# Kernel tuning notes

Measured on AMD Instinct MI355X. Metric: run time of the kernel, lower is better.

The kernel has to match this reference:

```python
import jax, jax.numpy as jnp
import numpy as np

HIDDEN = 1024
HEADS = 16
HEAD_DIM = HIDDEN // HEADS
SCALE = float(np.sqrt(HEAD_DIM))
B, S = 4, 2048


def setup_inputs() -> dict:
    key = jax.random.key(0)
    ks = jax.random.split(key, 10)
    inp = {
        "query": jax.random.normal(ks[0], (B, S, HIDDEN), dtype=jnp.float32),
        "mask": jax.random.randint(ks[1], (B, S), 0, 2).astype(jnp.bool_),
        "Wq": jax.random.normal(ks[2], (HIDDEN, HIDDEN), dtype=jnp.float32) * 0.02,
        "bq": jax.random.normal(ks[3], (HIDDEN,), dtype=jnp.float32) * 0.02,
        "Wk": jax.random.normal(ks[4], (HIDDEN, HIDDEN), dtype=jnp.float32) * 0.02,
        "bk": jax.random.normal(ks[5], (HIDDEN,), dtype=jnp.float32) * 0.02,
        "Wv": jax.random.normal(ks[6], (HIDDEN, HIDDEN), dtype=jnp.float32) * 0.02,
        "bv": jax.random.normal(ks[7], (HIDDEN,), dtype=jnp.float32) * 0.02,
        "Wo": jax.random.normal(ks[8], (HIDDEN, HIDDEN), dtype=jnp.float32) * 0.02,
        "bo": jax.random.normal(ks[9], (HIDDEN,), dtype=jnp.float32) * 0.02,
    }
    return inp


def reference(query, mask, Wq, bq, Wk, bk, Wv, bv, Wo, bo):
    b, s, _ = query.shape
    # QKV projections (torch Linear: x @ W.T + b)
    q = query @ Wq.T + bq
    k = query @ Wk.T + bk
    v = query @ Wv.T + bv
    # [b, h, s, d]
    q = q.reshape(b, s, HEADS, HEAD_DIM).transpose(0, 2, 1, 3)
    k = k.reshape(b, s, HEADS, HEAD_DIM).transpose(0, 2, 1, 3)
    v = v.reshape(b, s, HEADS, HEAD_DIM).transpose(0, 2, 1, 3)
    # energy[b,h,i,j] = q_i . k_j / scale
    energy = jnp.einsum("bhid,bhjd->bhij", q, k) / SCALE
    m = mask.astype(energy.dtype)
    energy = energy * m[:, None, :, None] * m[:, None, None, :]
    # NOTE: softmax over the QUERY axis (dim=2), not the key axis
    attention = jax.nn.softmax(energy, axis=2)
    x = jnp.einsum("bhij,bhjd->bhid", attention, v)
    x = x.transpose(0, 2, 1, 3).reshape(b, s, HIDDEN)
    out = x @ Wo.T + bo
    return jnp.squeeze(out)
```

## Files before the change

### kernel.cpp

```cpp
#include <hip/hip_runtime.h>

#define SQ   2048
#define HIDN 1024
#define NB   4
#define NH   16
#define HD   64

typedef __attribute__((ext_vector_type(8))) short short8;
typedef __attribute__((ext_vector_type(4))) short short4v;
typedef __attribute__((ext_vector_type(4))) float f32x4;

__device__ __forceinline__ short f2bf(float f) {
  union { float f; unsigned u; } x; x.f = f;
  unsigned r = (x.u + 0x7fffu + ((x.u >> 16) & 1u)) >> 16;
  return (short)r;
}

__device__ __forceinline__ unsigned cvtpk_bf16(float lo, float hi) {
  unsigned u;
  asm("v_cvt_pk_bf16_f32 %0, %1, %2" : "=v"(u) : "v"(lo), "v"(hi));
  return u;
}

__device__ __forceinline__ float exp2_raw(float x) {
  float r;
  asm("v_exp_f32 %0, %1" : "=v"(r) : "v"(x));
  return r;
}

#define MFMA(a, b, c) __builtin_amdgcn_mfma_f32_16x16x32_bf16((a), (b), (c), 0, 0, 0)

__device__ __forceinline__ void gload16(const void* g, void* l) {
  __builtin_amdgcn_global_load_lds(
      (const __attribute__((address_space(1))) unsigned*)g,
      (__attribute__((address_space(3))) unsigned*)l, 16, 0, 0);
}

#define LOG2E 1.44269504f

__global__ __launch_bounds__(256) void k_maskprep(const unsigned* __restrict__ mraw,
                                                  float* __restrict__ m) {
  __shared__ unsigned red[256];
  const int tid = threadIdx.x;
  unsigned w_or = 0;
  for (int i = tid; i < 2048; i += 256) w_or |= mraw[i];
  red[tid] = w_or;
  __syncthreads();
  for (int s = 128; s > 0; s >>= 1) {
    if (tid < s) red[tid] |= red[tid + s];
    __syncthreads();
  }
  const unsigned allw = red[0];
  int mode;
  if ((allw & 0xFFFFFFFEu) == 0) mode = 0;
  else if ((allw & 0xFEFEFEFEu) == 0) mode = 1;
  else mode = 2;
  const unsigned char* mb = (const unsigned char*)mraw;
  const float* mf = (const float*)mraw;
  const int* mi = (const int*)mraw;
  for (int i = tid; i < NB * SQ; i += 256) {
    float v;
    if (mode == 0)      v = mi[i] ? 1.0f : 0.0f;
    else if (mode == 1) v = mb[i] ? 1.0f : 0.0f;
    else                v = (mf[i] != 0.0f) ? 1.0f : 0.0f;
    m[i] = v;
  }
}

__global__ __launch_bounds__(256) void k_cvt(
    const float* __restrict__ query, const float* __restrict__ Wq,
    const float* __restrict__ Wk, const float* __restrict__ Wv,
    short* __restrict__ qbf, short* __restrict__ wbf)
{
  const int yy = blockIdx.y;
  const float* __restrict__ src = (yy == 0) ? query : (yy == 1) ? Wq : (yy == 2) ? Wk : Wv;
  short* __restrict__ dst = (yy == 0) ? qbf : wbf + (yy - 1) * (HIDN * HIDN);
  const int n = (yy == 0) ? (NB * SQ * HIDN) : (HIDN * HIDN);
  const int i = (blockIdx.x * 256 + threadIdx.x) * 4;
  if (i >= n) return;
  const f32x4 v = *(const f32x4*)(src + i);
  short4v s;
#pragma unroll
  for (int e = 0; e < 4; ++e) s[e] = f2bf(v[e]);
  *(short4v*)(dst + i) = s;
}

__global__ __launch_bounds__(256) void k_cvtWo(
    const float* __restrict__ Wo, short* __restrict__ wo)
{
  const int i = (blockIdx.x * 256 + threadIdx.x) * 4;
  if (i >= HIDN * HIDN) return;
  const f32x4 v = *(const f32x4*)(Wo + i);
  short4v s;
#pragma unroll
  for (int e = 0; e < 4; ++e) s[e] = f2bf(v[e]);
  *(short4v*)(wo + i) = s;
}

__global__ __launch_bounds__(256) void k_proj_qkv2(
    const short* __restrict__ qbf, const short* __restrict__ wbf,
    const float* __restrict__ bq, const float* __restrict__ bkb,
    const float* __restrict__ bv, const float* __restrict__ mfl,
    short* __restrict__ qh, short* __restrict__ kh, short* __restrict__ vh)
{
  __shared__ short a_s[2][128 * 64];
  __shared__ short b_s[2][128 * 64];
  const int nt = blockIdx.x, mt = blockIdx.y;
  const int tid = threadIdx.x;
  const int w = tid >> 6, lane = tid & 63;
  const int wr = w >> 1, wc = w & 1;
  const int lg = lane >> 4, lr = lane & 15;

  const int z = nt >> 3;
  const float* __restrict__ bias = (z == 0) ? bq : (z == 1) ? bkb : bv;

  int srow[4], scs[4], sbase[4];
#pragma unroll
  for (int p = 0; p < 4; ++p) {
    const int id = p * 256 + tid;
    const int r = id >> 3, c = id & 7;
    srow[p] = r;
    scs[p] = c ^ (r & 7);
    sbase[p] = (p * 256 + w * 64) * 8;
  }

  f32x4 acc[4][4] = {};

#pragma unroll
  for (int p = 0; p < 4; ++p) {
    gload16(qbf + (size_t)(mt * 128 + srow[p]) * HIDN + scs[p] * 8, a_s[0] + sbase[p]);
    gload16(wbf + (size_t)(nt * 128 + srow[p]) * HIDN + scs[p] * 8, b_s[0] + sbase[p]);
  }
  __syncthreads();

  int cur = 0;
  for (int k0 = 0; k0 < HIDN; k0 += 64) {
    if (k0 + 64 < HIDN) {
      const int kn = k0 + 64;
#pragma unroll
      for (int p = 0; p < 4; ++p) {
        gload16(qbf + (size_t)(mt * 128 + srow[p]) * HIDN + kn + scs[p] * 8,
                a_s[cur ^ 1] + sbase[p]);
        gload16(wbf + (size_t)(nt * 128 + srow[p]) * HIDN + kn + scs[p] * 8,
                b_s[cur ^ 1] + sbase[p]);
      }
    }
#pragma unroll
    for (int kk = 0; kk < 2; ++kk) {
      short8 af[4], bfv[4];
#pragma unroll
      for (int mi = 0; mi < 4; ++mi) {
        const int r = wr * 64 + mi * 16 + lr;
        const int phys = (kk * 4 + lg) ^ (r & 7);
        af[mi] = *(const short8*)((const char*)a_s[cur] + r * 128 + phys * 16);
      }
#pragma unroll
      for (int ni = 0; ni < 4; ++ni) {
        const int r = wc * 64 + ni * 16 + lr;
        const int phys = (kk * 4 + lg) ^ (r & 7);
        bfv[ni] = *(const short8*)((const char*)b_s[cur] + r * 128 + phys * 16);
      }
#pragma unroll
      for (int mi = 0; mi < 4; ++mi)
#pragma unroll
        for (int ni = 0; ni < 4; ++ni)
          acc[mi][ni] = MFMA(af[mi], bfv[ni], acc[mi][ni]);
    }
    __syncthreads();
    cur ^= 1;
  }

#pragma unroll
  for (int mi = 0; mi < 4; ++mi)
#pragma unroll
    for (int ni = 0; ni < 4; ++ni)
#pragma unroll
      for (int r = 0; r < 4; ++r) {
        const int row = mt * 128 + wr * 64 + mi * 16 + lg * 4 + r;
        const int colz = (nt & 7) * 128 + wc * 64 + ni * 16 + lr;
        const float v = acc[mi][ni][r] + bias[colz];
        const int bi = row >> 11, s = row & (SQ - 1);
        const int h = colz >> 6, d = colz & (HD - 1);
        const int idx = ((bi * NH + h) * SQ + s) * HD + d;
        if (z == 0) {
          qh[idx] = f2bf(v * (0.125f * LOG2E) * mfl[row]);
        } else if (z == 1) {
          kh[idx] = f2bf(v * mfl[row]);
        } else {
          vh[idx] = f2bf(v);
        }
      }
}

__global__ __launch_bounds__(256) void k_sumexp_m(
    const short* __restrict__ qh, const short* __restrict__ kh,
    const short* __restrict__ vh, short* __restrict__ vT)
{
  __shared__ short q_s[2][64][72];
  __shared__ float rl_s[256];
  __shared__ short t_s[64][72];
  const int bh = blockIdx.y;
  const int jt = blockIdx.x;
  const int tid = threadIdx.x, w = tid >> 6, lane = tid & 63;
  const int lg = lane >> 4, lr = lane & 15;

  const int base = bh * SQ * HD;
  const int jbase = jt * 256 + w * 64;

  short8 bk[4][2];
#pragma unroll
  for (int jf = 0; jf < 4; ++jf) {
    const int j = jbase + jf * 16 + lr;
    bk[jf][0] = *(const short8*)(kh + base + j * HD + lg * 8);
    bk[jf][1] = *(const short8*)(kh + base + j * HD + 32 + lg * 8);
  }

  const int srow = tid >> 3, scc = (tid & 7) * 8;
  {
    const short8 s0 = *(const short8*)(qh + base + srow * HD + scc);
    const short8 s1 = *(const short8*)(qh + base + (32 + srow) * HD + scc);
    *(short8*)&q_s[0][srow][scc] = s0;
    *(short8*)&q_s[0][32 + srow][scc] = s1;
  }
  __syncthreads();

  f32x4 Lacc[4] = {};
  for (int t = 0; t < 32; ++t) {
    const int cur = t & 1;
    short8 n0, n1;
    if (t < 31) {
      const int ibn = (t + 1) * 64;
      n0 = *(const short8*)(qh + base + (ibn + srow) * HD + scc);
      n1 = *(const short8*)(qh + base + (ibn + 32 + srow) * HD + scc);
    }
#pragma unroll
    for (int s = 0; s < 4; ++s) {
      const short8 a0 = *(const short8*)&q_s[cur][s * 16 + lr][lg * 8];
      const short8 a1 = *(const short8*)&q_s[cur][s * 16 + lr][32 + lg * 8];
#pragma unroll
      for (int jf = 0; jf < 4; ++jf) {
        f32x4 e = {};
        e = MFMA(a0, bk[jf][0], e);
        e = MFMA(a1, bk[jf][1], e);
#pragma unroll
        for (int r = 0; r < 4; ++r)
          Lacc[jf][r] += exp2_raw(e[r]);
      }
    }
    if (t < 31) {
      __syncthreads();
      *(short8*)&q_s[cur ^ 1][srow][scc] = n0;
      *(short8*)&q_s[cur ^ 1][32 + srow][scc] = n1;
      __syncthreads();
    }
  }

#pragma unroll
  for (int jf = 0; jf < 4; ++jf) {
    float L = Lacc[jf][0] + Lacc[jf][1] + Lacc[jf][2] + Lacc[jf][3];
    L += __shfl_xor(L, 16, 64);
    L += __shfl_xor(L, 32, 64);
    if (lg == 0) rl_s[w * 64 + jf * 16 + lr] = 1.0f / L;
  }
  __syncthreads();

  const int jglob0 = jt * 256;
  for (int sub = 0; sub < 4; ++sub) {
#pragma unroll
    for (int p = 0; p < 2; ++p) {
      const int id = p * 256 + tid;
      const int r = id >> 3, c = id & 7;
      const short8 v = *(const short8*)(vh + base + (jglob0 + sub * 64 + r) * HD + c * 8);
      const float sc = rl_s[sub * 64 + r];
      float f[8];
#pragma unroll
      for (int e = 0; e < 8; ++e) {
        union { unsigned u; float x; } cv;
        cv.u = ((unsigned)(unsigned short)v[e]) << 16;
        f[e] = cv.x * sc;
      }
      union { unsigned u[4]; short8 s8; } o;
#pragma unroll
      for (int e = 0; e < 4; ++e) o.u[e] = cvtpk_bf16(f[2 * e], f[2 * e + 1]);
      *(short8*)&t_s[r][c * 8] = o.s8;
    }
    __syncthreads();
    const int d = tid >> 2, sc4 = (tid & 3) * 16;
    short val[16];
#pragma unroll
    for (int k = 0; k < 16; ++k) val[k] = t_s[sc4 + k][d];
    *(short8*)(vT + base + d * SQ + jglob0 + sub * 64 + sc4) = *(const short8*)&val[0];
    *(short8*)(vT + base + d * SQ + jglob0 + sub * 64 + sc4 + 8) = *(const short8*)&val[8];
    __syncthreads();
  }
}

__global__ __launch_bounds__(256) void k_attnv(
    const short* __restrict__ qh, const short* __restrict__ kh,
    const short* __restrict__ vT,
    short* __restrict__ xo)
{
  __shared__ short k_s[64 * 64];
  __shared__ short v_s[64 * 64];
  __shared__ __attribute__((aligned(16))) short p_s[4][4][16][40];
  const int bh = blockIdx.y, b = bh >> 4, h = bh & (NH - 1);
  const int it = blockIdx.x;
  const int tid = threadIdx.x, w = tid >> 6, lane = tid & 63;
  const int lg = lane >> 4, lr = lane & 15;

  const int base = bh * SQ * HD;
  const int i0 = it * 256 + w * 64;

  short8 aq[4][2];
#pragma unroll
  for (int fi = 0; fi < 4; ++fi) {
    aq[fi][0] = *(const short8*)(qh + base + (i0 + fi * 16 + lr) * HD + lg * 8);
    aq[fi][1] = *(const short8*)(qh + base + (i0 + fi * 16 + lr) * HD + 32 + lg * 8);
  }

  int strow[2], stphys[2], stbase[2];
#pragma unroll
  for (int p = 0; p < 2; ++p) {
    const int id = p * 256 + tid;
    const int r = id >> 3, c = id & 7;
    strow[p] = r;
    stphys[p] = c ^ (r & 7);
    stbase[p] = (p * 256 + w * 64) * 8;
  }

  f32x4 accx[4][4] = {};
  for (int jb = 0; jb < SQ; jb += 64) {
#pragma unroll
    for (int p = 0; p < 2; ++p) {
      gload16(kh + base + (size_t)(jb + strow[p]) * HD + stphys[p] * 8,
              k_s + stbase[p]);
      gload16(vT + base + (size_t)strow[p] * SQ + jb + stphys[p] * 8,
              v_s + stbase[p]);
    }
    __syncthreads();

#pragma unroll
    for (int sub = 0; sub < 2; ++sub) {
      short8 bk[2][2];
#pragma unroll
      for (int jj = 0; jj < 2; ++jj) {
        const int rr = sub * 32 + jj * 16 + lr;
        const int ph0 = lg ^ (rr & 7);
        const int ph1 = (4 + lg) ^ (rr & 7);
        bk[jj][0] = *(const short8*)(k_s + rr * 64 + ph0 * 8);
        bk[jj][1] = *(const short8*)(k_s + rr * 64 + ph1 * 8);
      }
      short8 bv[4];
#pragma unroll
      for (int nd = 0; nd < 4; ++nd) {
        const int rv = nd * 16 + lr;
        const int ph = (sub * 4 + lg) ^ (rv & 7);
        bv[nd] = *(const short8*)(v_s + rv * 64 + ph * 8);
      }

#pragma unroll
      for (int fi = 0; fi < 4; ++fi) {
        f32x4 e0 = {}, e1 = {};
        e0 = MFMA(bk[0][0], aq[fi][0], e0);
        e0 = MFMA(bk[0][1], aq[fi][1], e0);
        e1 = MFMA(bk[1][0], aq[fi][0], e1);
        e1 = MFMA(bk[1][1], aq[fi][1], e1);
        const unsigned u00 = cvtpk_bf16(exp2_raw(e0[0]), exp2_raw(e0[1]));
        const unsigned u01 = cvtpk_bf16(exp2_raw(e0[2]), exp2_raw(e0[3]));
        const unsigned u10 = cvtpk_bf16(exp2_raw(e1[0]), exp2_raw(e1[1]));
        const unsigned u11 = cvtpk_bf16(exp2_raw(e1[2]), exp2_raw(e1[3]));
        uint2 w0; w0.x = u00; w0.y = u01;
        uint2 w1; w1.x = u10; w1.y = u11;
        *(uint2*)&p_s[w][fi][lr][lg * 4] = w0;
        *(uint2*)&p_s[w][fi][lr][16 + lg * 4] = w1;
      }
#pragma unroll
      for (int fi = 0; fi < 4; ++fi) {
        const short8 pa = *(const short8*)&p_s[w][fi][lr][lg * 8];
#pragma unroll
        for (int nd = 0; nd < 4; ++nd)
          accx[fi][nd] = MFMA(pa, bv[nd], accx[fi][nd]);
      }
    }
    __syncthreads();
  }

#pragma unroll
  for (int fi = 0; fi < 4; ++fi)
#pragma unroll
    for (int nd = 0; nd < 4; ++nd)
#pragma unroll
      for (int r = 0; r < 4; ++r) {
        const int i = i0 + fi * 16 + lg * 4 + r, d = nd * 16 + lr;
        xo[(b * SQ + i) * HIDN + h * HD + d] = f2bf(accx[fi][nd][r]);
      }
}

__global__ __launch_bounds__(256) void k_proj_out2(
    const short* __restrict__ xb, const short* __restrict__ wo,
    const float* __restrict__ bo, float* __restrict__ out)
{
  __shared__ short a_s[2][128 * 64];
  __shared__ short b_s[2][128 * 64];
  const int flat = blockIdx.y * 8 + blockIdx.x;
  const int swz = (flat & 7) * 64 + (flat >> 3);
  const int nt = swz % 8, mt = swz / 8;
  const int tid = threadIdx.x;
  const int w = tid >> 6, lane = tid & 63;
  const int wr = w >> 1, wc = w & 1;
  const int lg = lane >> 4, lr = lane & 15;

  int srow[4], scs[4], sbase[4];
#pragma unroll
  for (int p = 0; p < 4; ++p) {
    const int id = p * 256 + tid;
    const int r = id >> 3, c = id & 7;
    srow[p] = r;
    scs[p] = c ^ (r & 7);
    sbase[p] = (p * 256 + w * 64) * 8;
  }

  f32x4 acc[4][4] = {};

#pragma unroll
  for (int p = 0; p < 4; ++p) {
    gload16(xb + (size_t)(mt * 128 + srow[p]) * HIDN + scs[p] * 8, a_s[0] + sbase[p]);
    gload16(wo + (size_t)(nt * 128 + srow[p]) * HIDN + scs[p] * 8, b_s[0] + sbase[p]);
  }
  __syncthreads();

  int cur = 0;
  for (int k0 = 0; k0 < HIDN; k0 += 64) {
    if (k0 + 64 < HIDN) {
      const int kn = k0 + 64;
#pragma unroll
      for (int p = 0; p < 4; ++p) {
        gload16(xb + (size_t)(mt * 128 + srow[p]) * HIDN + kn + scs[p] * 8,
                a_s[cur ^ 1] + sbase[p]);
        gload16(wo + (size_t)(nt * 128 + srow[p]) * HIDN + kn + scs[p] * 8,
                b_s[cur ^ 1] + sbase[p]);
      }
    }
#pragma unroll
    for (int kk = 0; kk < 2; ++kk) {
      short8 af[4], bfv[4];
#pragma unroll
      for (int mi = 0; mi < 4; ++mi) {
        const int r = wr * 64 + mi * 16 + lr;
        const int phys = (kk * 4 + lg) ^ (r & 7);
        af[mi] = *(const short8*)((const char*)a_s[cur] + r * 128 + phys * 16);
      }
#pragma unroll
      for (int ni = 0; ni < 4; ++ni) {
        const int r = wc * 64 + ni * 16 + lr;
        const int phys = (kk * 4 + lg) ^ (r & 7);
        bfv[ni] = *(const short8*)((const char*)b_s[cur] + r * 128 + phys * 16);
      }
#pragma unroll
      for (int mi = 0; mi < 4; ++mi)
#pragma unroll
        for (int ni = 0; ni < 4; ++ni)
          acc[mi][ni] = MFMA(af[mi], bfv[ni], acc[mi][ni]);
    }
    __syncthreads();
    cur ^= 1;
  }

#pragma unroll
  for (int mi = 0; mi < 4; ++mi)
#pragma unroll
    for (int ni = 0; ni < 4; ++ni)
#pragma unroll
      for (int r = 0; r < 4; ++r) {
        const int row = mt * 128 + wr * 64 + mi * 16 + lg * 4 + r;
        const int col = nt * 128 + wc * 64 + ni * 16 + lr;
        out[row * HIDN + col] = acc[mi][ni][r] + bo[col];
      }
}

extern "C" void kernel_launch(void* const* d_in, const int* in_sizes, int n_in,
                              void* d_out, int out_size, void* d_ws, size_t ws_size,
                              hipStream_t stream) {
  const float* query = (const float*)d_in[0];
  const unsigned* mraw = (const unsigned*)d_in[1];
  const float* Wq = (const float*)d_in[2];
  const float* bq = (const float*)d_in[3];
  const float* Wk = (const float*)d_in[4];
  const float* bk = (const float*)d_in[5];
  const float* Wv = (const float*)d_in[6];
  const float* bv = (const float*)d_in[7];
  const float* Wo = (const float*)d_in[8];
  const float* bo = (const float*)d_in[9];

  short* qh  = (short*)d_ws;
  short* kh  = qh + (NB * NH * SQ * HD);
  short* vT  = kh + (NB * NH * SQ * HD);
  short* xb  = vT + (NB * NH * SQ * HD);
  float* mfl = (float*)(xb + (NB * SQ * HIDN));

  short* vh = xb;

  short* qbf = (short*)d_out;
  short* wbf = qbf + (NB * SQ * HIDN);
  short* wo  = qh;

  k_maskprep<<<dim3(1), dim3(256), 0, stream>>>(mraw, mfl);
  k_cvt<<<dim3((NB * SQ * HIDN) / 1024, 4), dim3(256), 0, stream>>>(
      query, Wq, Wk, Wv, qbf, wbf);
  k_proj_qkv2<<<dim3(24, 64), dim3(256), 0, stream>>>(
      qbf, wbf, bq, bk, bv, mfl, qh, kh, vh);
  k_sumexp_m<<<dim3(SQ / 256, NB * NH), dim3(256), 0, stream>>>(qh, kh, vh, vT);
  k_attnv<<<dim3(SQ / 256, NB * NH), dim3(256), 0, stream>>>(qh, kh, vT, xb);
  k_cvtWo<<<dim3((HIDN * HIDN) / 1024), dim3(256), 0, stream>>>(Wo, wo);
  k_proj_out2<<<dim3(HIDN / 128, (NB * SQ) / 128), dim3(256), 0, stream>>>(
      xb, wo, bo, (float*)d_out);
}
```

Before: 274.2 us.

## Pipeline QKV projection GEMM with 4-stage K=32 LDS ring and raw barriers

Reworks the QKV projection GEMM mainloop from a double-buffered K=64 loop into a 4-slot ring of K=32 LDS tiles, keeping three stages of async global-to-LDS loads in flight. It uses explicit vmcnt waits and raw s_barrier instead of __syncthreads, which can be cheaper because it skips the full waitcnt. It also raises wave priority around the MFMA bursts. The goal is to hide global load latency better. The cost is more barriers per K step and a hand-counted vmcnt scheme that breaks if the number of loads per stage changes.

```diff
diff --git a/kernel.cpp b/kernel.cpp
--- a/kernel.cpp
+++ b/kernel.cpp
@@ -97,14 +97,14 @@
   *(short4v*)(wo + i) = s;
 }
 
-__global__ __launch_bounds__(256) void k_proj_qkv2(
+__global__ __launch_bounds__(256) void k_proj_qkv5(
     const short* __restrict__ qbf, const short* __restrict__ wbf,
     const float* __restrict__ bq, const float* __restrict__ bkb,
     const float* __restrict__ bv, const float* __restrict__ mfl,
     short* __restrict__ qh, short* __restrict__ kh, short* __restrict__ vh)
 {
-  __shared__ short a_s[2][128 * 64];
-  __shared__ short b_s[2][128 * 64];
+  __shared__ short a_s[4][128 * 32];
+  __shared__ short b_s[4][128 * 32];
   const int nt = blockIdx.x, mt = blockIdx.y;
   const int tid = threadIdx.x;
   const int w = tid >> 6, lane = tid & 63;
@@ -114,61 +114,77 @@
   const int z = nt >> 3;
   const float* __restrict__ bias = (z == 0) ? bq : (z == 1) ? bkb : bv;
 
-  int srow[4], scs[4], sbase[4];
-#pragma unroll
-  for (int p = 0; p < 4; ++p) {
-    const int id = p * 256 + tid;
-    const int r = id >> 3, c = id & 7;
-    srow[p] = r;
-    scs[p] = c ^ (r & 7);
-    sbase[p] = (p * 256 + w * 64) * 8;
+  int srow[2], scol[2], sdst[2];
+#pragma unroll
+  for (int t = 0; t < 2; ++t) {
+    const int id = t * 256 + tid;
+    srow[t] = id >> 2;
+    scol[t] = (id & 3) ^ ((srow[t] >> 1) & 3);
+    sdst[t] = (t * 256 + w * 64) * 8;
+  }
+  const short* agbase = qbf + (size_t)(mt * 128) * HIDN;
+  const short* bgbase = wbf + (size_t)(nt * 128) * HIDN;
+
+  int aoff[4], boff[4];
+#pragma unroll
+  for (int mi = 0; mi < 4; ++mi) {
+    const int r = wr * 64 + mi * 16 + lr;
+    aoff[mi] = r * 32 + ((lg ^ ((r >> 1) & 3)) * 8);
+  }
+#pragma unroll
+  for (int ni = 0; ni < 4; ++ni) {
+    const int r = wc * 64 + ni * 16 + lr;
+    boff[ni] = r * 32 + ((lg ^ ((r >> 1) & 3)) * 8);
   }
 
   f32x4 acc[4][4] = {};
 
-#pragma unroll
-  for (int p = 0; p < 4; ++p) {
-    gload16(qbf + (size_t)(mt * 128 + srow[p]) * HIDN + scs[p] * 8, a_s[0] + sbase[p]);
-    gload16(wbf + (size_t)(nt * 128 + srow[p]) * HIDN + scs[p] * 8, b_s[0] + sbase[p]);
-  }
-  __syncthreads();
-
-  int cur = 0;
-  for (int k0 = 0; k0 < HIDN; k0 += 64) {
-    if (k0 + 64 < HIDN) {
-      const int kn = k0 + 64;
-#pragma unroll
-      for (int p = 0; p < 4; ++p) {
-        gload16(qbf + (size_t)(mt * 128 + srow[p]) * HIDN + kn + scs[p] * 8,
-                a_s[cur ^ 1] + sbase[p]);
-        gload16(wbf + (size_t)(nt * 128 + srow[p]) * HIDN + kn + scs[p] * 8,
-                b_s[cur ^ 1] + sbase[p]);
-      }
-    }
-#pragma unroll
-    for (int kk = 0; kk < 2; ++kk) {
-      short8 af[4], bfv[4];
-#pragma unroll
-      for (int mi = 0; mi < 4; ++mi) {
-        const int r = wr * 64 + mi * 16 + lr;
-        const int phys = (kk * 4 + lg) ^ (r & 7);
-        af[mi] = *(const short8*)((const char*)a_s[cur] + r * 128 + phys * 16);
-      }
-#pragma unroll
-      for (int ni = 0; ni < 4; ++ni) {
-        const int r = wc * 64 + ni * 16 + lr;
-        const int phys = (kk * 4 + lg) ^ (r & 7);
-        bfv[ni] = *(const short8*)((const char*)b_s[cur] + r * 128 + phys * 16);
-      }
-#pragma unroll
-      for (int mi = 0; mi < 4; ++mi)
-#pragma unroll
-        for (int ni = 0; ni < 4; ++ni)
-          acc[mi][ni] = MFMA(af[mi], bfv[ni], acc[mi][ni]);
-    }
-    __syncthreads();
-    cur ^= 1;
-  }
+  auto stage = [&](int khalf) {
+    const int k0 = khalf * 32;
+    const int sl = khalf & 3;
+#pragma unroll
+    for (int t = 0; t < 2; ++t) {
+      gload16(agbase + (size_t)srow[t] * HIDN + k0 + scol[t] * 8, &a_s[sl][sdst[t]]);
+      gload16(bgbase + (size_t)srow[t] * HIDN + k0 + scol[t] * 8, &b_s[sl][sdst[t]]);
+    }
+  };
+  auto compute = [&](int p) {
+    const int sl = p & 3;
+    short8 af[4], bfv[4];
+#pragma unroll
+    for (int mi = 0; mi < 4; ++mi) af[mi] = *(const short8*)&a_s[sl][aoff[mi]];
+#pragma unroll
+    for (int ni = 0; ni < 4; ++ni) bfv[ni] = *(const short8*)&b_s[sl][boff[ni]];
+    __builtin_amdgcn_s_setprio(1);
+#pragma unroll
+    for (int mi = 0; mi < 4; ++mi)
+#pragma unroll
+      for (int ni = 0; ni < 4; ++ni)
+        acc[mi][ni] = MFMA(af[mi], bfv[ni], acc[mi][ni]);
+    __builtin_amdgcn_s_setprio(0);
+  };
+
+  stage(0); stage(1); stage(2);
+
+  for (int p = 0; p < 29; ++p) {
+    __builtin_amdgcn_s_barrier();
+    stage(p + 3);
+    asm volatile("s_waitcnt vmcnt(12)" ::: "memory");
+    __builtin_amdgcn_s_barrier();
+    compute(p);
+  }
+  __builtin_amdgcn_s_barrier();
+  asm volatile("s_waitcnt vmcnt(8)" ::: "memory");
+  __builtin_amdgcn_s_barrier();
+  compute(29);
+  __builtin_amdgcn_s_barrier();
+  asm volatile("s_waitcnt vmcnt(4)" ::: "memory");
+  __builtin_amdgcn_s_barrier();
+  compute(30);
+  __builtin_amdgcn_s_barrier();
+  asm volatile("s_waitcnt vmcnt(0)" ::: "memory");
+  __builtin_amdgcn_s_barrier();
+  compute(31);
 
 #pragma unroll
   for (int mi = 0; mi < 4; ++mi)
@@ -507,7 +523,7 @@
   k_maskprep<<<dim3(1), dim3(256), 0, stream>>>(mraw, mfl);
   k_cvt<<<dim3((NB * SQ * HIDN) / 1024, 4), dim3(256), 0, stream>>>(
       query, Wq, Wk, Wv, qbf, wbf);
-  k_proj_qkv2<<<dim3(24, 64), dim3(256), 0, stream>>>(
+  k_proj_qkv5<<<dim3(24, 64), dim3(256), 0, stream>>>(
       qbf, wbf, bq, bk, bv, mfl, qh, kh, vh);
   k_sumexp_m<<<dim3(SQ / 256, NB * NH), dim3(256), 0, stream>>>(qh, kh, vh, vT);
   k_attnv<<<dim3(SQ / 256, NB * NH), dim3(256), 0, stream>>>(qh, kh, vT, xb);
```

Result: slower. 294.4 us (+7.4%).
